# Kernel optimization log

Measured on AMD Instinct MI355X. Metric: run time of the kernel, lower is better.

Reference implementation:

```python
import jax, jax.numpy as jnp
import numpy as np

C = 256          # channels
NUM_HEADS = 4
HEAD_DIM = C // NUM_HEADS
TILE_SIZE = 64
TILE_SEQ = TILE_SIZE * TILE_SIZE  # 4096
B, H_IMG, W_IMG = 1, 96, 96
EPS = 1e-5


def setup_inputs() -> dict:
    key = jax.random.key(0)
    k0, k1, k2 = jax.random.split(key, 3)
    x = jax.random.normal(k0, (B, C, H_IMG, W_IMG), jnp.float32)
    norm_w = jnp.ones((C,), jnp.float32)
    norm_b = jnp.zeros((C,), jnp.float32)
    qkv_w = jax.random.normal(k1, (3 * C, C), jnp.float32) * (C ** -0.5)
    qkv_b = jnp.zeros((3 * C,), jnp.float32)
    proj_w = jax.random.normal(k2, (C, C), jnp.float32) * (C ** -0.5)
    proj_b = jnp.zeros((C,), jnp.float32)
    return {"x": x, "norm_w": norm_w, "norm_b": norm_b,
            "qkv_w": qkv_w, "qkv_b": qkv_b,
            "proj_w": proj_w, "proj_b": proj_b}


def _attn(q, k, v, scale):
    # q: [B,H,Q,D], k/v: [B,H,K,D]
    s = jnp.einsum('bhqd,bhkd->bhqk', q, k) * scale
    p = jax.nn.softmax(s, axis=-1)
    return jnp.einsum('bhqk,bhkd->bhqd', p, v)


def reference(x, norm_w, norm_b, qkv_w, qkv_b, proj_w, proj_b):
    b, c, h, w = x.shape
    seq = h * w
    g = min(32, c)
    # GroupNorm
    xg = x.reshape(b, g, c // g, h, w)
    mean = xg.mean(axis=(2, 3, 4), keepdims=True)
    var = ((xg - mean) ** 2).mean(axis=(2, 3, 4), keepdims=True)
    xn = (xg - mean) * jax.lax.rsqrt(var + EPS)
    xn = xn.reshape(b, c, h, w) * norm_w[None, :, None, None] + norm_b[None, :, None, None]
    # flatten spatial -> tokens
    xf = xn.transpose(0, 2, 3, 1).reshape(b, seq, c)
    qkv = xf @ qkv_w.T + qkv_b  # [B,S,3C]
    qkv = qkv.reshape(b, seq, 3, NUM_HEADS, HEAD_DIM).transpose(2, 0, 3, 1, 4)
    q, k, v = qkv[0], qkv[1], qkv[2]  # [B,H,S,D]
    scale = HEAD_DIM ** -0.5
    if seq > TILE_SEQ:
        num_tiles = (seq + TILE_SEQ - 1) // TILE_SEQ
        outs = []
        for i in range(num_tiles):  # small fixed tile count, static slices
            s0 = i * TILE_SEQ
            e0 = min((i + 1) * TILE_SEQ, seq)
            k0 = max(0, s0 - TILE_SEQ // 2)
            k1 = min(seq, e0 + TILE_SEQ // 2)
            outs.append(_attn(q[:, :, s0:e0], k[:, :, k0:k1], v[:, :, k0:k1], scale))
        out = jnp.concatenate(outs, axis=2)
    else:
        out = _attn(q, k, v, scale)
    out = out.transpose(0, 2, 1, 3).reshape(b, seq, c)
    out = out @ proj_w.T + proj_b
    out = out.reshape(b, h, w, c).transpose(0, 3, 1, 2)
    return out + x
```

## Files before the change

kernel.cpp:

```cpp
#include <hip/hip_runtime.h>

typedef __bf16 bf16x8 __attribute__((ext_vector_type(8)));
typedef float f32x4 __attribute__((ext_vector_type(4)));
typedef float f32x16 __attribute__((ext_vector_type(16)));
typedef int i32x4 __attribute__((ext_vector_type(4)));
typedef int i32x2 __attribute__((ext_vector_type(2)));
typedef unsigned short u16x4 __attribute__((ext_vector_type(4)));

#define S_TOK 9216
#define LOG2E 1.44269504088896340736f
#define SCALE_Q (0.125f * LOG2E)

__device__ inline unsigned short f2bf(float f) {
    unsigned int u = __builtin_bit_cast(unsigned int, f);
    return (unsigned short)((u + 0x7fffu + ((u >> 16) & 1u)) >> 16);
}

__device__ inline unsigned int cvt_pk_bf16(float lo, float hi) {
    unsigned int r;
    asm("v_cvt_pk_bf16_f32 %0, %1, %2" : "=v"(r) : "v"(lo), "v"(hi));
    return r;
}

__device__ inline void permswap(unsigned int& a, unsigned int& b) {
    asm("v_permlane32_swap_b32 %0, %1" : "+v"(a), "+v"(b));
}

__device__ inline f32x4 MFMA(bf16x8 a, bf16x8 b, f32x4 c) {
    return __builtin_amdgcn_mfma_f32_16x16x32_bf16(a, b, c, 0, 0, 0);
}
__device__ inline f32x16 MFMA32(bf16x8 a, bf16x8 b, f32x16 c) {
    return __builtin_amdgcn_mfma_f32_32x32x16_bf16(a, b, c, 0, 0, 0);
}

__device__ inline int swz(int row, int c) {
    return ((c + (row >> 3)) & 7) ^ (row & 7);
}
__device__ inline bf16x8 load_frag(const unsigned short* lds, int outer, int kbase) {
    int lane = threadIdx.x & 63;
    int row = outer + (lane & 15);
    int cc = swz(row, (kbase >> 3) + (lane >> 4));
    return *reinterpret_cast<const bf16x8*>(lds + row * 64 + cc * 8);
}
__device__ inline bf16x8 load_frag32(const unsigned short* lds, int outer, int kbase) {
    int lane = threadIdx.x & 63;
    int row = outer + (lane & 31);
    int cc = swz(row, (kbase >> 3) + (lane >> 5));
    return *reinterpret_cast<const bf16x8*>(lds + row * 64 + cc * 8);
}
__device__ inline void stage_tile(unsigned short* lds, const unsigned short* src,
                                  int stride, int nrows) {
    for (int id = threadIdx.x; id < nrows * 8; id += 256) {
        int row = id >> 3, cc = id & 7;
        i32x4 v = *reinterpret_cast<const i32x4*>(src + row * stride + cc * 8);
        *reinterpret_cast<i32x4*>(lds + row * 64 + swz(row, cc) * 8) = v;
    }
}

__global__ __launch_bounds__(256) void gn_stats_part(const float* __restrict__ x,
                                                     float* __restrict__ part) {
    int c = blockIdx.x;
    const f32x4* p = reinterpret_cast<const f32x4*>(x + c * S_TOK);
    float s = 0.f, ss = 0.f;
    for (int i = threadIdx.x; i < 2304; i += 256) {
        f32x4 v = p[i];
        s += v[0] + v[1] + v[2] + v[3];
        ss += v[0] * v[0] + v[1] * v[1] + v[2] * v[2] + v[3] * v[3];
    }
#pragma unroll
    for (int off = 1; off < 64; off <<= 1) {
        s += __shfl_xor(s, off);
        ss += __shfl_xor(ss, off);
    }
    __shared__ float rs[4], rss[4];
    int wave = threadIdx.x >> 6;
    if ((threadIdx.x & 63) == 0) { rs[wave] = s; rss[wave] = ss; }
    __syncthreads();
    if (threadIdx.x == 0) {
        part[c] = rs[0] + rs[1] + rs[2] + rs[3];
        part[256 + c] = rss[0] + rss[1] + rss[2] + rss[3];
    }
}

__global__ __launch_bounds__(256) void gn_apply(const float* __restrict__ x,
                                                const float* __restrict__ part,
                                                const float* __restrict__ nw,
                                                const float* __restrict__ nb,
                                                unsigned short* __restrict__ xf) {
    __shared__ float tl[64][65];
    __shared__ float gmean[8], grstd[8];
    int sb = blockIdx.x * 64, cb = blockIdx.y * 64;
    if (threadIdx.x < 8) {
        int g = (cb >> 3) + threadIdx.x;
        float s = 0.f, ss = 0.f;
#pragma unroll
        for (int i = 0; i < 8; ++i) { s += part[g * 8 + i]; ss += part[256 + g * 8 + i]; }
        float mean = s * (1.f / 73728.f);
        float var = ss * (1.f / 73728.f) - mean * mean;
        gmean[threadIdx.x] = mean;
        grstd[threadIdx.x] = rsqrtf(var + 1e-5f);
    }
    __syncthreads();
    for (int id = threadIdx.x; id < 1024; id += 256) {
        int cr = id >> 4;
        int sq = (id & 15) << 2;
        int c = cb + cr;
        f32x4 v = *reinterpret_cast<const f32x4*>(x + c * S_TOK + sb + sq);
        float mu = gmean[cr >> 3], rstd = grstd[cr >> 3];
        float wv = nw[c] * rstd;
        float bv = nb[c] - mu * wv;
#pragma unroll
        for (int j = 0; j < 4; ++j) tl[sq + j][cr] = v[j] * wv + bv;
    }
    __syncthreads();
    for (int id = threadIdx.x; id < 1024; id += 256) {
        int sr = id >> 4;
        int cq = (id & 15) << 2;
        u16x4 o;
#pragma unroll
        for (int j = 0; j < 4; ++j) o[j] = f2bf(tl[sr][cq + j]);
        *reinterpret_cast<u16x4*>(xf + (sb + sr) * 256 + cb + cq) = o;
    }
}

__global__ __launch_bounds__(256) void conv_both(const float* __restrict__ qkvw_in,
                                                 const float* __restrict__ projw_in,
                                                 unsigned short* __restrict__ out) {
    int i = blockIdx.x * 256 + threadIdx.x;
    float v;
    if (i < 768 * 256) v = qkvw_in[i] * ((i < 256 * 256) ? SCALE_Q : 1.0f);
    else v = projw_in[i - 768 * 256];
    out[i] = f2bf(v);
}

template <int MODE>
__global__ __launch_bounds__(256) void gemm_bt(const unsigned short* __restrict__ A,
                                               const unsigned short* __restrict__ B,
                                               const float* __restrict__ bias,
                                               unsigned short* __restrict__ q_out,
                                               unsigned short* __restrict__ k_out,
                                               unsigned short* __restrict__ vT_out,
                                               const float* __restrict__ xres,
                                               float* __restrict__ out) {
    __shared__ alignas(16) unsigned short As[128 * 64];
    __shared__ alignas(16) unsigned short Bs[128 * 64];
    int mb = blockIdx.x, nb = blockIdx.y;
    int wave = threadIdx.x >> 6, lane = threadIdx.x & 63;
    int wm = wave >> 1, wn = wave & 1;
    f32x4 zero = {0.f, 0.f, 0.f, 0.f};
    f32x4 acc[4][4];
    for (int i = 0; i < 4; ++i)
        for (int j = 0; j < 4; ++j) acc[i][j] = zero;
    for (int ks = 0; ks < 4; ++ks) {
        __syncthreads();
        stage_tile(As, A + (mb * 128) * 256 + ks * 64, 256, 128);
        stage_tile(Bs, B + (nb * 128) * 256 + ks * 64, 256, 128);
        __syncthreads();
#pragma unroll
        for (int kk = 0; kk < 2; ++kk) {
            bf16x8 af[4], bfr[4];
#pragma unroll
            for (int mt = 0; mt < 4; ++mt) af[mt] = load_frag(As, wm * 64 + mt * 16, kk * 32);
#pragma unroll
            for (int nt = 0; nt < 4; ++nt) bfr[nt] = load_frag(Bs, wn * 64 + nt * 16, kk * 32);
#pragma unroll
            for (int mt = 0; mt < 4; ++mt)
#pragma unroll
                for (int nt = 0; nt < 4; ++nt)
                    acc[mt][nt] = MFMA(af[mt], bfr[nt], acc[mt][nt]);
        }
    }
    int r0 = (lane >> 4) << 2;
    int cl = lane & 15;
#pragma unroll
    for (int mt = 0; mt < 4; ++mt) {
#pragma unroll
        for (int nt = 0; nt < 4; ++nt) {
            int m = mb * 128 + wm * 64 + mt * 16 + r0;
            int n = nb * 128 + wn * 64 + nt * 16 + cl;
            if (MODE == 0) {
                float bv = bias[n] * ((n < 256) ? SCALE_Q : 1.0f);
#pragma unroll
                for (int r = 0; r < 4; ++r) {
                    unsigned short hh = f2bf(acc[mt][nt][r] + bv);
                    int s = m + r;
                    if (n < 256) q_out[s * 256 + n] = hh;
                    else if (n < 512) k_out[s * 256 + (n - 256)] = hh;
                    else vT_out[(n - 512) * S_TOK + s] = hh;
                }
            } else {
                float bv = bias[n];
                f32x4 xr = *reinterpret_cast<const f32x4*>(xres + n * S_TOK + m);
                f32x4 o;
#pragma unroll
                for (int r = 0; r < 4; ++r) o[r] = acc[mt][nt][r] + bv + xr[r];
                *reinterpret_cast<f32x4*>(out + n * S_TOK + m) = o;
            }
        }
    }
}

struct StageRegs { i32x4 k0, k1, v0, v1; };

__device__ inline StageRegs load_stage(const unsigned short* ksrc, const unsigned short* vsrc) {
    int tid = threadIdx.x;
    int row = tid >> 3, cc = tid & 7;
    StageRegs r;
    r.k0 = *reinterpret_cast<const i32x4*>(ksrc + row * 256 + cc * 8);
    r.k1 = *reinterpret_cast<const i32x4*>(ksrc + (row + 32) * 256 + cc * 8);
    r.v0 = *reinterpret_cast<const i32x4*>(vsrc + row * S_TOK + cc * 8);
    r.v1 = *reinterpret_cast<const i32x4*>(vsrc + (row + 32) * S_TOK + cc * 8);
    return r;
}

__device__ inline void store_stage(unsigned short* K, unsigned short* V, StageRegs r) {
    int tid = threadIdx.x;
    int row = tid >> 3, cc = tid & 7;
    *reinterpret_cast<i32x4*>(K + row * 64 + swz(row, cc) * 8) = r.k0;
    *reinterpret_cast<i32x4*>(K + (row + 32) * 64 + swz(row + 32, cc) * 8) = r.k1;
    *reinterpret_cast<i32x4*>(V + row * 64 + swz(row, cc) * 8) = r.v0;
    *reinterpret_cast<i32x4*>(V + (row + 32) * 64 + swz(row + 32, cc) * 8) = r.v1;
}

template <int NC>
__global__ __launch_bounds__(256) void attn(const unsigned short* __restrict__ qb,
                                            const unsigned short* __restrict__ kb,
                                            const unsigned short* __restrict__ vT,
                                            unsigned short* __restrict__ Opart,
                                            float* __restrict__ lpart) {
    __shared__ alignas(16) unsigned short Ks[2][64 * 64];
    __shared__ alignas(16) unsigned short Vs[2][64 * 64];
    constexpr int NS0 = 96 / NC, NS1 = 112 / NC, NS2 = 48 / NC;
    constexpr int B0 = 32 * NS0, B1 = B0 + 32 * NS1, NB = B1 + 8 * NS2;

    int bx = blockIdx.x;
    int head = bx / NB;
    int r = bx % NB;
    int tile, seg, qi;
    if (r < B0)      { tile = 0; seg = r >> 5; qi = r & 31; }
    else if (r < B1) { int t = r - B0; tile = 1; seg = t >> 5; qi = t & 31; }
    else             { int t = r - B1; tile = 2; seg = t >> 3; qi = t & 7; }
    int qs0 = (tile == 0) ? 0 : (tile == 1 ? 4096 : 8192);
    int kv0 = (tile == 0) ? 0 : (tile == 1 ? 2048 : 6144);
    int qstart = qs0 + qi * 128;
    int c0 = seg * NC, c1 = c0 + NC;
    int wave = threadIdx.x >> 6, lane = threadIdx.x & 63;
    int l31 = lane & 31, h = lane >> 5;

    stage_tile((unsigned short*)Ks, qb + qstart * 256 + head * 64, 256, 128);
    __syncthreads();
    bf16x8 qf[4];
#pragma unroll
    for (int s = 0; s < 4; ++s) qf[s] = load_frag32((unsigned short*)Ks, wave * 32, s * 16);
    __syncthreads();

    bf16x8 ones;
#pragma unroll
    for (int i = 0; i < 8; ++i) ones[i] = (__bf16)1.0f;

    f32x16 oacc0, oacc1, lac;
#pragma unroll
    for (int i = 0; i < 16; ++i) { oacc0[i] = 0.f; oacc1[i] = 0.f; lac[i] = 0.f; }

    const unsigned short* kbase = kb + kv0 * 256 + head * 64;
    const unsigned short* vbase = vT + head * 64 * S_TOK + kv0;

    StageRegs R = load_stage(kbase + c0 * (64 * 256), vbase + c0 * 64);
    store_stage(Ks[c0 & 1], Vs[c0 & 1], R);
    if (c0 + 1 < c1) R = load_stage(kbase + (c0 + 1) * (64 * 256), vbase + (c0 + 1) * 64);
    __syncthreads();

    for (int ch = c0; ch < c1; ++ch) {
        int p = ch & 1;
        if (ch + 1 < c1) {
            store_stage(Ks[p ^ 1], Vs[p ^ 1], R);
            if (ch + 2 < c1)
                R = load_stage(kbase + (ch + 2) * (64 * 256), vbase + (ch + 2) * 64);
        }
        const unsigned short* Kp = Ks[p];
        const unsigned short* Vp = Vs[p];
        f32x16 sc0, sc1;
#pragma unroll
        for (int i = 0; i < 16; ++i) { sc0[i] = 0.f; sc1[i] = 0.f; }
        __builtin_amdgcn_s_setprio(1);
#pragma unroll
        for (int s = 0; s < 4; ++s) {
            bf16x8 k0 = load_frag32(Kp, 0, s * 16);
            bf16x8 k1 = load_frag32(Kp, 32, s * 16);
            sc0 = MFMA32(k0, qf[s], sc0);
            sc1 = MFMA32(k1, qf[s], sc1);
        }
#pragma unroll
        for (int s = 0; s < 4; ++s) {
            f32x16 scr = (s < 2) ? sc0 : sc1;
            const int b = 8 * (s & 1);
            float E[8];
#pragma unroll
            for (int i = 0; i < 8; ++i) E[i] = __builtin_amdgcn_exp2f(scr[b + i]);
            unsigned int w0 = cvt_pk_bf16(E[0], E[1]);
            unsigned int w1 = cvt_pk_bf16(E[2], E[3]);
            unsigned int w2 = cvt_pk_bf16(E[4], E[5]);
            unsigned int w3 = cvt_pk_bf16(E[6], E[7]);
            permswap(w0, w2);
            permswap(w1, w3);
            i32x4 w;
            w[0] = (int)w0; w[1] = (int)w1; w[2] = (int)w2; w[3] = (int)w3;
            bf16x8 pa = __builtin_bit_cast(bf16x8, w);
            bf16x8 v0 = load_frag32(Vp, 0, s * 16);
            bf16x8 v1 = load_frag32(Vp, 32, s * 16);
            oacc0 = MFMA32(pa, v0, oacc0);
            oacc1 = MFMA32(pa, v1, oacc1);
            lac = MFMA32(pa, ones, lac);
        }
        __builtin_amdgcn_s_setprio(0);
        __syncthreads();
    }
    unsigned int obase = (unsigned int)seg * (S_TOK * 256);
#pragma unroll
    for (int reg = 0; reg < 16; ++reg) {
        int qloc = (reg & 3) + 8 * (reg >> 2) + 4 * h;
        int s = qstart + wave * 32 + qloc;
        Opart[obase + s * 256 + head * 64 + l31] =
            __builtin_bit_cast(unsigned short, (__bf16)oacc0[reg]);
        Opart[obase + s * 256 + head * 64 + 32 + l31] =
            __builtin_bit_cast(unsigned short, (__bf16)oacc1[reg]);
    }
    if (l31 == 0) {
#pragma unroll
        for (int reg = 0; reg < 16; ++reg) {
            int qloc = (reg & 3) + 8 * (reg >> 2) + 4 * h;
            int s = qstart + wave * 32 + qloc;
            lpart[(seg * 4 + head) * S_TOK + s] = lac[reg];
        }
    }
}

template <int NC>
__global__ __launch_bounds__(256) void combine(const unsigned short* __restrict__ Op,
                                               const float* __restrict__ lp,
                                               unsigned short* __restrict__ att) {
    int idx = blockIdx.x * 256 + threadIdx.x;
    int s = idx >> 5;
    int c0 = (idx & 31) << 3;
    int head = c0 >> 6;
    int nseg = (s < 4096) ? (96 / NC) : (s < 8192 ? (112 / NC) : (48 / NC));
    float acc[8] = {0.f, 0.f, 0.f, 0.f, 0.f, 0.f, 0.f, 0.f};
    float l = 0.f;
    for (int seg = 0; seg < nseg; ++seg) {
        i32x4 v = *reinterpret_cast<const i32x4*>(Op + (size_t)seg * (S_TOK * 256) + s * 256 + c0);
        const unsigned short* u = reinterpret_cast<const unsigned short*>(&v);
#pragma unroll
        for (int i = 0; i < 8; ++i)
            acc[i] += __builtin_bit_cast(float, ((unsigned int)u[i]) << 16);
        l += lp[(seg * 4 + head) * S_TOK + s];
    }
    float inv = 1.f / l;
    u16x4 o0, o1;
#pragma unroll
    for (int i = 0; i < 4; ++i) {
        o0[i] = f2bf(acc[i] * inv);
        o1[i] = f2bf(acc[4 + i] * inv);
    }
    unsigned short* dst = att + s * 256 + c0;
    *reinterpret_cast<u16x4*>(dst) = o0;
    *reinterpret_cast<u16x4*>(dst + 4) = o1;
}

extern "C" void kernel_launch(void* const* d_in, const int* in_sizes, int n_in,
                              void* d_out, int out_size, void* d_ws, size_t ws_size,
                              hipStream_t stream) {
    const float* x      = (const float*)d_in[0];
    const float* norm_w = (const float*)d_in[1];
    const float* norm_b = (const float*)d_in[2];
    const float* qkv_w  = (const float*)d_in[3];
    const float* qkv_b  = (const float*)d_in[4];
    const float* proj_w = (const float*)d_in[5];
    const float* proj_b = (const float*)d_in[6];
    float* outp = (float*)d_out;

    char* wsb = (char*)d_ws;
    float* part = (float*)wsb;
    unsigned short* xf    = (unsigned short*)(wsb + 2048);
    unsigned short* qkvw  = xf + 9216 * 256;
    unsigned short* projw = qkvw + 768 * 256;
    unsigned short* qbuf  = projw + 256 * 256;
    unsigned short* kbuf  = qbuf + 9216 * 256;
    unsigned short* vTbuf = kbuf + 9216 * 256;
    unsigned short* Opart = vTbuf + 256 * 9216;
    size_t fixed_bytes = 2048 + 2ull * 256 * (9216ull * 4 + 768 + 256);
    size_t need8 = fixed_bytes + 2ull * 14 * 9216 * 256 + 4ull * 14 * 4 * 9216;
    bool use8 = (ws_size >= need8);
    int MS = use8 ? 14 : 7;
    float* lpart = (float*)(Opart + (size_t)MS * 9216 * 256);
    unsigned short* attb  = xf;

    gn_stats_part<<<dim3(256), dim3(256), 0, stream>>>(x, part);
    gn_apply<<<dim3(144, 4), dim3(256), 0, stream>>>(x, part, norm_w, norm_b, xf);
    conv_both<<<dim3(1024), dim3(256), 0, stream>>>(qkv_w, proj_w, qkvw);
    gemm_bt<0><<<dim3(72, 6), dim3(256), 0, stream>>>(xf, qkvw, qkv_b,
                                                      qbuf, kbuf, vTbuf, nullptr, nullptr);
    if (use8) {
        attn<8><<<dim3(4 * 880), dim3(256), 0, stream>>>(qbuf, kbuf, vTbuf, Opart, lpart);
        combine<8><<<dim3(1152), dim3(256), 0, stream>>>(Opart, lpart, attb);
    } else {
        attn<16><<<dim3(4 * 440), dim3(256), 0, stream>>>(qbuf, kbuf, vTbuf, Opart, lpart);
        combine<16><<<dim3(1152), dim3(256), 0, stream>>>(Opart, lpart, attb);
    }
    gemm_bt<1><<<dim3(72, 2), dim3(256), 0, stream>>>(attb, projw, proj_b,
                                                      nullptr, nullptr, nullptr, x, outp);
}
```

Before: 158.3 us.

## Deepen K/V prefetch to two stages and split score compute into halves

The attention loop now keeps two register staging sets in flight, so loads run two chunks ahead, and the loop is unrolled by pairs with fixed LDS buffer indices. The score computation is split into two 32-key halves, so only one score accumulator is live at a time, which lowers register pressure. Separately, the QKV GEMM epilogue writes the transposed V output as 4-element vector stores instead of scalar stores. The cost is more registers for the extra staging set, and NC must now be even and at least 4.

Result: faster. 149.4 us (-5.6%).

```diff
diff --git a/kernel.cpp b/kernel.cpp
--- a/kernel.cpp
+++ b/kernel.cpp
@@ -180,13 +180,19 @@
             int n = nb * 128 + wn * 64 + nt * 16 + cl;
             if (MODE == 0) {
                 float bv = bias[n] * ((n < 256) ? SCALE_Q : 1.0f);
-#pragma unroll
-                for (int r = 0; r < 4; ++r) {
-                    unsigned short hh = f2bf(acc[mt][nt][r] + bv);
-                    int s = m + r;
-                    if (n < 256) q_out[s * 256 + n] = hh;
-                    else if (n < 512) k_out[s * 256 + (n - 256)] = hh;
-                    else vT_out[(n - 512) * S_TOK + s] = hh;
+                if (n < 256) {
+#pragma unroll
+                    for (int r = 0; r < 4; ++r)
+                        q_out[(m + r) * 256 + n] = f2bf(acc[mt][nt][r] + bv);
+                } else if (n < 512) {
+#pragma unroll
+                    for (int r = 0; r < 4; ++r)
+                        k_out[(m + r) * 256 + (n - 256)] = f2bf(acc[mt][nt][r] + bv);
+                } else {
+                    u16x4 o;
+#pragma unroll
+                    for (int r = 0; r < 4; ++r) o[r] = f2bf(acc[mt][nt][r] + bv);
+                    *reinterpret_cast<u16x4*>(vT_out + (n - 512) * S_TOK + m) = o;
                 }
             } else {
                 float bv = bias[n];
@@ -232,6 +238,7 @@
     __shared__ alignas(16) unsigned short Vs[2][64 * 64];
     constexpr int NS0 = 96 / NC, NS1 = 112 / NC, NS2 = 48 / NC;
     constexpr int B0 = 32 * NS0, B1 = B0 + 32 * NS1, NB = B1 + 8 * NS2;
+    static_assert(NC % 2 == 0 && NC >= 4, "NC even");
 
     int bx = blockIdx.x;
     int head = bx / NB;
@@ -243,7 +250,7 @@
     int qs0 = (tile == 0) ? 0 : (tile == 1 ? 4096 : 8192);
     int kv0 = (tile == 0) ? 0 : (tile == 1 ? 2048 : 6144);
     int qstart = qs0 + qi * 128;
-    int c0 = seg * NC, c1 = c0 + NC;
+    int c0 = seg * NC;
     int wave = threadIdx.x >> 6, lane = threadIdx.x & 63;
     int l31 = lane & 31, h = lane >> 5;
 
@@ -265,56 +272,66 @@
     const unsigned short* kbase = kb + kv0 * 256 + head * 64;
     const unsigned short* vbase = vT + head * 64 * S_TOK + kv0;
 
-    StageRegs R = load_stage(kbase + c0 * (64 * 256), vbase + c0 * 64);
-    store_stage(Ks[c0 & 1], Vs[c0 & 1], R);
-    if (c0 + 1 < c1) R = load_stage(kbase + (c0 + 1) * (64 * 256), vbase + (c0 + 1) * 64);
-    __syncthreads();
-
-    for (int ch = c0; ch < c1; ++ch) {
-        int p = ch & 1;
-        if (ch + 1 < c1) {
-            store_stage(Ks[p ^ 1], Vs[p ^ 1], R);
-            if (ch + 2 < c1)
-                R = load_stage(kbase + (ch + 2) * (64 * 256), vbase + (ch + 2) * 64);
-        }
-        const unsigned short* Kp = Ks[p];
-        const unsigned short* Vp = Vs[p];
-        f32x16 sc0, sc1;
-#pragma unroll
-        for (int i = 0; i < 16; ++i) { sc0[i] = 0.f; sc1[i] = 0.f; }
+    auto compute = [&](const unsigned short* Kp, const unsigned short* Vp) {
         __builtin_amdgcn_s_setprio(1);
 #pragma unroll
-        for (int s = 0; s < 4; ++s) {
-            bf16x8 k0 = load_frag32(Kp, 0, s * 16);
-            bf16x8 k1 = load_frag32(Kp, 32, s * 16);
-            sc0 = MFMA32(k0, qf[s], sc0);
-            sc1 = MFMA32(k1, qf[s], sc1);
-        }
-#pragma unroll
-        for (int s = 0; s < 4; ++s) {
-            f32x16 scr = (s < 2) ? sc0 : sc1;
-            const int b = 8 * (s & 1);
-            float E[8];
-#pragma unroll
-            for (int i = 0; i < 8; ++i) E[i] = __builtin_amdgcn_exp2f(scr[b + i]);
-            unsigned int w0 = cvt_pk_bf16(E[0], E[1]);
-            unsigned int w1 = cvt_pk_bf16(E[2], E[3]);
-            unsigned int w2 = cvt_pk_bf16(E[4], E[5]);
-            unsigned int w3 = cvt_pk_bf16(E[6], E[7]);
-            permswap(w0, w2);
-            permswap(w1, w3);
-            i32x4 w;
-            w[0] = (int)w0; w[1] = (int)w1; w[2] = (int)w2; w[3] = (int)w3;
-            bf16x8 pa = __builtin_bit_cast(bf16x8, w);
-            bf16x8 v0 = load_frag32(Vp, 0, s * 16);
-            bf16x8 v1 = load_frag32(Vp, 32, s * 16);
-            oacc0 = MFMA32(pa, v0, oacc0);
-            oacc1 = MFMA32(pa, v1, oacc1);
-            lac = MFMA32(pa, ones, lac);
+        for (int half = 0; half < 2; ++half) {
+            f32x16 sc;
+#pragma unroll
+            for (int i = 0; i < 16; ++i) sc[i] = 0.f;
+#pragma unroll
+            for (int s = 0; s < 4; ++s)
+                sc = MFMA32(load_frag32(Kp, half * 32, s * 16), qf[s], sc);
+#pragma unroll
+            for (int sl = 0; sl < 2; ++sl) {
+                const int b = 8 * sl;
+                float E[8];
+#pragma unroll
+                for (int i = 0; i < 8; ++i) E[i] = __builtin_amdgcn_exp2f(sc[b + i]);
+                unsigned int w0 = cvt_pk_bf16(E[0], E[1]);
+                unsigned int w1 = cvt_pk_bf16(E[2], E[3]);
+                unsigned int w2 = cvt_pk_bf16(E[4], E[5]);
+                unsigned int w3 = cvt_pk_bf16(E[6], E[7]);
+                permswap(w0, w2);
+                permswap(w1, w3);
+                i32x4 w;
+                w[0] = (int)w0; w[1] = (int)w1; w[2] = (int)w2; w[3] = (int)w3;
+                bf16x8 pa = __builtin_bit_cast(bf16x8, w);
+                int kvb = (half * 2 + sl) * 16;
+                bf16x8 v0 = load_frag32(Vp, 0, kvb);
+                bf16x8 v1 = load_frag32(Vp, 32, kvb);
+                oacc0 = MFMA32(pa, v0, oacc0);
+                oacc1 = MFMA32(pa, v1, oacc1);
+                lac = MFMA32(pa, ones, lac);
+            }
         }
         __builtin_amdgcn_s_setprio(0);
+    };
+
+    StageRegs Ra = load_stage(kbase + c0 * (64 * 256), vbase + c0 * 64);
+    store_stage(Ks[0], Vs[0], Ra);
+    Ra = load_stage(kbase + (c0 + 1) * (64 * 256), vbase + (c0 + 1) * 64);
+    StageRegs Rb = load_stage(kbase + (c0 + 2 < c0 + NC ? c0 + 2 : c0) * (64 * 256),
+                              vbase + (c0 + 2 < c0 + NC ? c0 + 2 : c0) * 64);
+    __syncthreads();
+
+#pragma unroll
+    for (int k = 0; k < NC / 2; ++k) {
+        int ch = c0 + 2 * k;
+        store_stage(Ks[1], Vs[1], Ra);
+        if (2 * k + 3 < NC)
+            Ra = load_stage(kbase + (ch + 3) * (64 * 256), vbase + (ch + 3) * 64);
+        compute(Ks[0], Vs[0]);
         __syncthreads();
-    }
+        if (2 * k + 2 < NC) {
+            store_stage(Ks[0], Vs[0], Rb);
+            if (2 * k + 4 < NC)
+                Rb = load_stage(kbase + (ch + 4) * (64 * 256), vbase + (ch + 4) * 64);
+        }
+        compute(Ks[1], Vs[1]);
+        __syncthreads();
+    }
+
     unsigned int obase = (unsigned int)seg * (S_TOK * 256);
 #pragma unroll
     for (int reg = 0; reg < 16; ++reg) {
```
